# Performance work log

Measured on AMD Instinct MI355X. Metric: run time of the kernel, lower is better.

## Reference

```python
import jax, jax.numpy as jnp
import numpy as np

N, E, F, H, C = 50000, 800000, 64, 64, 10


def setup_inputs() -> dict:
    key = jax.random.key(0)
    ks = jax.random.split(key, 9)
    x = jax.random.normal(ks[0], (N, F), dtype=jnp.float32)
    edge_index = jax.random.randint(ks[1], (2, E), 0, N, dtype=jnp.int64)
    s_f = 1.0 / np.sqrt(F)
    s_h = 1.0 / np.sqrt(H)
    return {
        "x": x,
        "edge_index": edge_index,
        # ChebConv(F->H, K=1): only Theta_0
        "W1_0": jax.random.normal(ks[2], (F, H), dtype=jnp.float32) * s_f,
        "b1": jnp.zeros((H,), dtype=jnp.float32),
        # ChebConv(H->H, K=2): Theta_0, Theta_1
        "W2_0": jax.random.normal(ks[3], (H, H), dtype=jnp.float32) * s_h,
        "W2_1": jax.random.normal(ks[4], (H, H), dtype=jnp.float32) * s_h,
        "b2": jnp.zeros((H,), dtype=jnp.float32),
        # final Linear(H->C)
        "Wl": jax.random.normal(ks[5], (H, C), dtype=jnp.float32) * s_h,
        "bl": jnp.zeros((C,), dtype=jnp.float32),
    }


def reference(x, edge_index, W1_0, b1, W2_0, W2_1, b2, Wl, bl):
    n = x.shape[0]
    src, dst = edge_index[0], edge_index[1]
    # Scaled Laplacian (PyG ChebConv, sym norm, lambda_max=2.0):
    # L_hat = -D^{-1/2} A D^{-1/2}  (self-loop terms cancel: +1 scaled, then -1 added)
    deg = jax.ops.segment_sum(jnp.ones((src.shape[0],), dtype=x.dtype), src,
                              num_segments=n)
    dis = jnp.where(deg > 0, jax.lax.rsqrt(jnp.maximum(deg, 1.0)), 0.0)
    w = -(dis[src] * dis[dst])  # [E]

    def lap(h):  # L_hat @ h via edge-wise gather/scatter
        return jax.ops.segment_sum(w[:, None] * h[src], dst, num_segments=n)

    # conv1 (K=1): T0 = x only -> plain linear
    h = jax.nn.relu(x @ W1_0 + b1)
    # dropout is identity in eval mode
    x_res = h
    # conv2 (K=2): T0 = h, T1 = L_hat h
    h2 = jax.nn.relu(h @ W2_0 + lap(h) @ W2_1 + b2)
    out = (h2 + x_res) @ Wl + bl
    return jax.nn.log_softmax(out, axis=1)
```

## Files before the change

kernel.cpp:

```cpp
#include <hip/hip_runtime.h>
#include <math.h>
#include <stdint.h>


#define NBKT 256
#define BCAP 5120
#define CHUNK 2048

__device__ __forceinline__ unsigned short f2bf(float f) {
    uint32_t u; __builtin_memcpy(&u, &f, 4);
    u += 0x7fffu + ((u >> 16) & 1u);
    return (unsigned short)(u >> 16);
}
__device__ __forceinline__ float bf2f(unsigned short s) {
    uint32_t u = (uint32_t)s << 16; float f; __builtin_memcpy(&f, &u, 4);
    return f;
}
__device__ __forceinline__ int xcc_id() {
    int x;
    asm("s_getreg_b32 %0, hwreg(HW_REG_XCC_ID)" : "=s"(x));
    return x;
}

__global__ __launch_bounds__(256) void binA_kernel(const int* __restrict__ ei,
                                                   int* __restrict__ gcur,
                                                   uint32_t* __restrict__ pairs,
                                                   int* __restrict__ degI8,
                                                   int E, int n) {
    __shared__ uint32_t stage[CHUNK];
    __shared__ int cnt[NBKT], obase[NBKT], goff[NBKT], curs[NBKT];
    __shared__ int wpart[4], stot;
    int t = threadIdx.x, lane = t & 63, wv = t >> 6;
    int e0 = blockIdx.x * CHUNK;
    int* degP = degI8 + (size_t)(xcc_id() & 7) * n;
    int s[8], d[8];
    bool val[8];
#pragma unroll
    for (int j = 0; j < 8; ++j) {
        int e = e0 + j * 256 + t;
        val[j] = e < E;
        s[j] = val[j] ? ei[e] : 0;
        d[j] = val[j] ? ei[E + e] : 0;
    }
    cnt[t] = 0;
    __syncthreads();
#pragma unroll
    for (int j = 0; j < 8; ++j)
        if (val[j]) {
            atomicAdd(&cnt[d[j] >> 8], 1);
            atomicAdd(&degP[s[j]], 1);
        }
    __syncthreads();
    int cv = cnt[t];
    int v = cv;
#pragma unroll
    for (int dd = 1; dd < 64; dd <<= 1) {
        int u = __shfl_up(v, dd);
        if (lane >= dd) v += u;
    }
    if (lane == 63) wpart[wv] = v;
    __syncthreads();
    if (t == 0) {
        int r = 0;
#pragma unroll
        for (int w = 0; w < 4; ++w) { int tmp = wpart[w]; wpart[w] = r; r += tmp; }
        stot = r;
    }
    __syncthreads();
    int eb = wpart[wv] + v - cv;
    obase[t] = eb;
    curs[t] = eb;
    goff[t] = (cv > 0) ? atomicAdd(&gcur[t], cv) : 0;
    __syncthreads();
#pragma unroll
    for (int j = 0; j < 8; ++j)
        if (val[j]) {
            int b = d[j] >> 8;
            int pos = atomicAdd(&curs[b], 1);
            stage[pos] = ((uint32_t)d[j] << 16) | (uint32_t)s[j];
        }
    __syncthreads();
    int tot = stot;
    for (int k = t; k < tot; k += 256) {
        uint32_t u = stage[k];
        int b = (int)(u >> 24);
        int slot = goff[b] + (k - obase[b]);
        if (slot < BCAP) pairs[(size_t)b * BCAP + slot] = u;
    }
}

__global__ __launch_bounds__(256) void binB_kernel(const int* __restrict__ gcur,
                                                   const uint32_t* __restrict__ pairs,
                                                   int* __restrict__ csr,
                                                   int* __restrict__ rowptr,
                                                   int* __restrict__ cntD,
                                                   int* __restrict__ cntLow,
                                                   const int* __restrict__ degI8,
                                                   float* __restrict__ dis,
                                                   int n, int half) {
    __shared__ int hist[NBKT], obase[NBKT], cursL[NBKT], cursH[NBKT];
    __shared__ int wpart[4];
    int t = threadIdx.x, lane = t & 63, wv = t >> 6;
    int b = blockIdx.x;
    {
        int node = b * 256 + t;
        if (node < n) {
            int dsum = 0;
#pragma unroll
            for (int j = 0; j < 8; ++j) dsum += degI8[(size_t)j * n + node];
            dis[node] = (dsum > 0) ? rsqrtf((float)dsum) : 0.0f;
        }
    }
    int nb = gcur[b]; if (nb > BCAP) nb = BCAP;
    hist[t] = 0;
    __syncthreads();
    const uint32_t* bp = pairs + (size_t)b * BCAP;
    for (int k = t; k < nb; k += 256) {
        int ld = (int)((bp[k] >> 16) & 255);
        atomicAdd(&hist[ld], 1);
    }
    __syncthreads();
    int cv = hist[t];
    int v = cv;
#pragma unroll
    for (int dd = 1; dd < 64; dd <<= 1) {
        int u = __shfl_up(v, dd);
        if (lane >= dd) v += u;
    }
    if (lane == 63) wpart[wv] = v;
    __syncthreads();
    if (t == 0) {
        int r = 0;
#pragma unroll
        for (int w = 0; w < 4; ++w) { int tmp = wpart[w]; wpart[w] = r; r += tmp; }
    }
    __syncthreads();
    int eb = wpart[wv] + v - cv;
    obase[t] = eb;
    cursL[t] = eb;
    cursH[t] = eb + cv;
    int node = b * 256 + t;
    if (node < n) {
        rowptr[node] = b * BCAP + eb;
        cntD[node] = cv;
    }
    __syncthreads();
    for (int k = t; k < nb; k += 256) {
        uint32_t u = bp[k];
        int ld = (int)((u >> 16) & 255);
        int src = (int)(u & 0xffffu);
        int pos;
        if (src < half) pos = atomicAdd(&cursL[ld], 1);
        else            pos = atomicSub(&cursH[ld], 1) - 1;
        csr[(size_t)b * BCAP + pos] = src;
    }
    __syncthreads();
    if (node < n) cntLow[node] = cursL[t] - obase[t];
}

__global__ __launch_bounds__(256) void gemm3_kernel(const float* __restrict__ x,
                                                    const float* __restrict__ W1,
                                                    const float* __restrict__ b1,
                                                    const float* __restrict__ W20,
                                                    const float* __restrict__ W21,
                                                    const float* __restrict__ b2,
                                                    const float* __restrict__ dis,
                                                    unsigned short* __restrict__ h16,
                                                    unsigned short* __restrict__ p16,
                                                    unsigned short* __restrict__ g16,
                                                    int n) {
    __shared__ __align__(16) float sA[64][68];
    __shared__ __align__(16) float sW1[64][64];
    __shared__ __align__(16) float sW20[64][64];
    __shared__ __align__(16) float sW21[64][64];
    int t = threadIdx.x;
    for (int i = t; i < 4096; i += 256) {
        sW1[i >> 6][i & 63] = W1[i];
        sW20[i >> 6][i & 63] = W20[i];
        sW21[i >> 6][i & 63] = W21[i];
    }
    int r0 = blockIdx.x * 64;
    {
        int rr0 = t >> 4, k0 = (t & 15) * 4;
        for (int rr = rr0; rr < 64; rr += 16) {
            int grow = r0 + rr;
            float4 v = make_float4(0.f, 0.f, 0.f, 0.f);
            if (grow < n) v = *(const float4*)&x[(size_t)grow * 64 + k0];
            sA[k0][rr] = v.x; sA[k0 + 1][rr] = v.y;
            sA[k0 + 2][rr] = v.z; sA[k0 + 3][rr] = v.w;
        }
    }
    __syncthreads();
    int tr = t >> 4, tc = t & 15;

    float acc[4][4] = {};
    for (int k = 0; k < 64; ++k) {
        float4 a = *(const float4*)&sA[k][tr * 4];
        float4 b = *(const float4*)&sW1[k][tc * 4];
        float av[4] = {a.x, a.y, a.z, a.w};
        float bv[4] = {b.x, b.y, b.z, b.w};
#pragma unroll
        for (int i = 0; i < 4; ++i)
#pragma unroll
            for (int j = 0; j < 4; ++j) acc[i][j] = fmaf(av[i], bv[j], acc[i][j]);
    }
    float4 bv1 = *(const float4*)&b1[tc * 4];
    float hv[4][4];
#pragma unroll
    for (int i = 0; i < 4; ++i) {
        hv[i][0] = fmaxf(acc[i][0] + bv1.x, 0.f);
        hv[i][1] = fmaxf(acc[i][1] + bv1.y, 0.f);
        hv[i][2] = fmaxf(acc[i][2] + bv1.z, 0.f);
        hv[i][3] = fmaxf(acc[i][3] + bv1.w, 0.f);
    }
#pragma unroll
    for (int i = 0; i < 4; ++i) {
        int grow = r0 + tr * 4 + i;
        if (grow < n) {
            ushort4 o;
            o.x = f2bf(hv[i][0]); o.y = f2bf(hv[i][1]);
            o.z = f2bf(hv[i][2]); o.w = f2bf(hv[i][3]);
            *(ushort4*)&h16[(size_t)grow * 64 + tc * 4] = o;
        }
    }
    __syncthreads();
#pragma unroll
    for (int i = 0; i < 4; ++i)
#pragma unroll
        for (int j = 0; j < 4; ++j) sA[tc * 4 + j][tr * 4 + i] = hv[i][j];
    __syncthreads();

    float accP[4][4] = {}, accG[4][4] = {};
    for (int k = 0; k < 64; ++k) {
        float4 a = *(const float4*)&sA[k][tr * 4];
        float4 bp = *(const float4*)&sW20[k][tc * 4];
        float4 bg = *(const float4*)&sW21[k][tc * 4];
        float av[4] = {a.x, a.y, a.z, a.w};
        float bpv[4] = {bp.x, bp.y, bp.z, bp.w};
        float bgv[4] = {bg.x, bg.y, bg.z, bg.w};
#pragma unroll
        for (int i = 0; i < 4; ++i)
#pragma unroll
            for (int j = 0; j < 4; ++j) {
                accP[i][j] = fmaf(av[i], bpv[j], accP[i][j]);
                accG[i][j] = fmaf(av[i], bgv[j], accG[i][j]);
            }
    }
    float4 bv2 = *(const float4*)&b2[tc * 4];
#pragma unroll
    for (int i = 0; i < 4; ++i) {
        int grow = r0 + tr * 4 + i;
        if (grow < n) {
            float dr = dis[grow];
            ushort4 op, og;
            op.x = f2bf(accP[i][0] + bv2.x); op.y = f2bf(accP[i][1] + bv2.y);
            op.z = f2bf(accP[i][2] + bv2.z); op.w = f2bf(accP[i][3] + bv2.w);
            og.x = f2bf(dr * accG[i][0]); og.y = f2bf(dr * accG[i][1]);
            og.z = f2bf(dr * accG[i][2]); og.w = f2bf(dr * accG[i][3]);
            *(ushort4*)&p16[(size_t)grow * 64 + tc * 4] = op;
            *(ushort4*)&g16[(size_t)grow * 64 + tc * 4] = og;
        }
    }
}

#define GATHER_SEG(K0, K1)                                                  \
    {                                                                        \
        int k = (K0);                                                        \
        for (; k + 16 <= (K1); k += 16) {                                    \
            int s0 = csr[rs + k],      s1 = csr[rs + k + 1];                 \
            int s2 = csr[rs + k + 2],  s3 = csr[rs + k + 3];                 \
            int s4 = csr[rs + k + 4],  s5 = csr[rs + k + 5];                 \
            int s6 = csr[rs + k + 6],  s7 = csr[rs + k + 7];                 \
            int s8 = csr[rs + k + 8],  s9 = csr[rs + k + 9];                 \
            int sa = csr[rs + k + 10], sb = csr[rs + k + 11];                \
            int sc = csr[rs + k + 12], sd = csr[rs + k + 13];                \
            int se = csr[rs + k + 14], sf = csr[rs + k + 15];                \
            float v0 = bf2f(g16[(size_t)s0 * 64 + c]);                       \
            float v1 = bf2f(g16[(size_t)s1 * 64 + c]);                       \
            float v2 = bf2f(g16[(size_t)s2 * 64 + c]);                       \
            float v3 = bf2f(g16[(size_t)s3 * 64 + c]);                       \
            float v4 = bf2f(g16[(size_t)s4 * 64 + c]);                       \
            float v5 = bf2f(g16[(size_t)s5 * 64 + c]);                       \
            float v6 = bf2f(g16[(size_t)s6 * 64 + c]);                       \
            float v7 = bf2f(g16[(size_t)s7 * 64 + c]);                       \
            float v8 = bf2f(g16[(size_t)s8 * 64 + c]);                       \
            float v9 = bf2f(g16[(size_t)s9 * 64 + c]);                       \
            float va = bf2f(g16[(size_t)sa * 64 + c]);                       \
            float vb = bf2f(g16[(size_t)sb * 64 + c]);                       \
            float vc = bf2f(g16[(size_t)sc * 64 + c]);                       \
            float vd = bf2f(g16[(size_t)sd * 64 + c]);                       \
            float ve = bf2f(g16[(size_t)se * 64 + c]);                       \
            float vf = bf2f(g16[(size_t)sf * 64 + c]);                       \
            a0 += v0 + v8; a1 += v1 + v9; a2 += v2 + va; a3 += v3 + vb;      \
            a4 += v4 + vc; a5 += v5 + vd; a6 += v6 + ve; a7 += v7 + vf;      \
        }                                                                    \
        for (; k + 4 <= (K1); k += 4) {                                      \
            int s0 = csr[rs + k],     s1 = csr[rs + k + 1];                  \
            int s2 = csr[rs + k + 2], s3 = csr[rs + k + 3];                  \
            a0 += bf2f(g16[(size_t)s0 * 64 + c]);                            \
            a1 += bf2f(g16[(size_t)s1 * 64 + c]);                            \
            a2 += bf2f(g16[(size_t)s2 * 64 + c]);                            \
            a3 += bf2f(g16[(size_t)s3 * 64 + c]);                            \
        }                                                                    \
        for (; k < (K1); ++k) {                                              \
            int s0 = csr[rs + k];                                            \
            a0 += bf2f(g16[(size_t)s0 * 64 + c]);                            \
        }                                                                    \
    }

__global__ __launch_bounds__(256, 8) void gather_out_kernel(
        const int* __restrict__ rowptr, const int* __restrict__ cntD,
        const int* __restrict__ cntLow, const int* __restrict__ csr,
        const float* __restrict__ dis,
        const unsigned short* __restrict__ g16, const unsigned short* __restrict__ p16,
        const unsigned short* __restrict__ h16, const float* __restrict__ Wl,
        const float* __restrict__ bl, float* __restrict__ out, int n) {
    __shared__ __align__(16) float so[4][68];
    __shared__ __align__(16) float sWlT[10][68];
    __shared__ float sout[4][12];
    int t = threadIdx.x;
    if (t < 160) {
        float4 w = *(const float4*)&Wl[t * 4];
        int i0 = t * 4;
        sWlT[i0 % 10][i0 / 10] = w.x;
        sWlT[(i0 + 1) % 10][(i0 + 1) / 10] = w.y;
        sWlT[(i0 + 2) % 10][(i0 + 2) / 10] = w.z;
        sWlT[(i0 + 3) % 10][(i0 + 3) / 10] = w.w;
    }
    int c = t & 63;
    int wid = __builtin_amdgcn_readfirstlane(t >> 6);
    int row = blockIdx.x * 4 + wid;
    if (row < n) {
        int m = cntD[row], rs = rowptr[row], mL = cntLow[row];
        float disd = dis[row];
        float a0 = 0.f, a1 = 0.f, a2 = 0.f, a3 = 0.f;
        float a4 = 0.f, a5 = 0.f, a6 = 0.f, a7 = 0.f;
        GATHER_SEG(0, mL);
        GATHER_SEG(mL, m);
        float lv = -disd * (((a0 + a1) + (a2 + a3)) + ((a4 + a5) + (a6 + a7)));
        float pv = bf2f(p16[(size_t)row * 64 + c]);
        float hv = bf2f(h16[(size_t)row * 64 + c]);
        so[wid][c] = fmaxf(pv + lv, 0.f) + hv;
    }
    __syncthreads();
    if (t < 40) {
        int r = t / 10, j = t % 10;
        float acc = bl[j];
#pragma unroll
        for (int k0 = 0; k0 < 64; k0 += 4) {
            float4 a = *(const float4*)&so[r][k0];
            float4 b = *(const float4*)&sWlT[j][k0];
            acc = fmaf(a.x, b.x, acc);
            acc = fmaf(a.y, b.y, acc);
            acc = fmaf(a.z, b.z, acc);
            acc = fmaf(a.w, b.w, acc);
        }
        sout[r][j] = acc;
    }
    __syncthreads();
    if (t < 64) {
        int r = t >> 4, l16 = t & 15;
        float v = (l16 < 10) ? sout[r][l16] : -1e30f;
        float mm = v;
#pragma unroll
        for (int d = 1; d < 16; d <<= 1) mm = fmaxf(mm, __shfl_xor(mm, d, 16));
        float e = (l16 < 10) ? expf(v - mm) : 0.f;
        float ss = e;
#pragma unroll
        for (int d = 1; d < 16; d <<= 1) ss += __shfl_xor(ss, d, 16);
        int grow = blockIdx.x * 4 + r;
        if (grow < n && l16 < 10)
            out[(size_t)grow * 10 + l16] = v - mm - logf(ss);
    }
}

extern "C" void kernel_launch(void* const* d_in, const int* in_sizes, int n_in,
                              void* d_out, int out_size, void* d_ws, size_t ws_size,
                              hipStream_t stream) {
    const float* x   = (const float*)d_in[0];
    const int*   ei  = (const int*)d_in[1];
    const float* W1  = (const float*)d_in[2];
    const float* b1  = (const float*)d_in[3];
    const float* W20 = (const float*)d_in[4];
    const float* W21 = (const float*)d_in[5];
    const float* b2  = (const float*)d_in[6];
    const float* Wl  = (const float*)d_in[7];
    const float* bl  = (const float*)d_in[8];
    float* out = (float*)d_out;

    int n = in_sizes[0] / 64;
    int E = in_sizes[1] / 2;

    char* ws = (char*)d_ws;
    size_t off = 0;
    auto alloc = [&](size_t bytes) {
        void* p = ws + off;
        off = (off + bytes + 255) & ~(size_t)255;
        return p;
    };
    int*       gcur   = (int*)alloc((size_t)NBKT * 4);
    uint32_t*  pairs  = (uint32_t*)alloc((size_t)NBKT * BCAP * 4);
    int*       csr    = (int*)alloc((size_t)NBKT * BCAP * 4);
    int*       rowptr = (int*)alloc((size_t)n * 4);
    int*       cntD   = (int*)alloc((size_t)n * 4);
    int*       cntLow = (int*)alloc((size_t)n * 4);
    int*       degI8  = (int*)alloc((size_t)n * 8 * 4);
    float*     dis    = (float*)alloc((size_t)n * 4);
    unsigned short* h16 = (unsigned short*)alloc((size_t)n * 64 * 2);
    unsigned short* p16 = (unsigned short*)alloc((size_t)n * 64 * 2);
    unsigned short* g16 = (unsigned short*)alloc((size_t)n * 64 * 2);

    hipMemsetAsync(gcur, 0, (size_t)NBKT * 4, stream);
    hipMemsetAsync(degI8, 0, (size_t)n * 8 * 4, stream);

    int nchunk = (E + CHUNK - 1) / CHUNK;
    binA_kernel<<<nchunk, 256, 0, stream>>>(ei, gcur, pairs, degI8, E, n);
    binB_kernel<<<NBKT, 256, 0, stream>>>(gcur, pairs, csr, rowptr, cntD, cntLow,
                                          degI8, dis, n, n / 2);
    gemm3_kernel<<<(n + 63) / 64, 256, 0, stream>>>(x, W1, b1, W20, W21, b2, dis,
                                                    h16, p16, g16, n);
    gather_out_kernel<<<(n + 3) / 4, 256, 0, stream>>>(rowptr, cntD, cntLow, csr,
                                                       dis, g16, p16, h16, Wl, bl,
                                                       out, n);
}
```

Baseline: 198.5 us.

## Gather two bf16 features per lane with half-waves splitting edges

The gather kernel now reads packed bf16 pairs as 32-bit words, so each half-wave covers a full 64-feature row. The two half-waves process alternating edges and combine their sums with a cross-lane shuffle. This halves the number of load instructions per edge and doubles the edges in flight per wave. The low/high source split in CSR construction (cntLow, the two-ended cursors) is dropped in favour of a single cursor, which gives up the locality ordering of source indices that the split provided.

```diff
diff --git a/kernel.cpp b/kernel.cpp
--- a/kernel.cpp
+++ b/kernel.cpp
@@ -15,6 +15,12 @@
 __device__ __forceinline__ float bf2f(unsigned short s) {
     uint32_t u = (uint32_t)s << 16; float f; __builtin_memcpy(&f, &u, 4);
     return f;
+}
+__device__ __forceinline__ float lo_of(uint32_t u) {
+    uint32_t v = u << 16; float f; __builtin_memcpy(&f, &v, 4); return f;
+}
+__device__ __forceinline__ float hi_of(uint32_t u) {
+    uint32_t v = u & 0xffff0000u; float f; __builtin_memcpy(&f, &v, 4); return f;
 }
 __device__ __forceinline__ int xcc_id() {
     int x;
@@ -94,11 +100,9 @@
                                                    int* __restrict__ csr,
                                                    int* __restrict__ rowptr,
                                                    int* __restrict__ cntD,
-                                                   int* __restrict__ cntLow,
                                                    const int* __restrict__ degI8,
-                                                   float* __restrict__ dis,
-                                                   int n, int half) {
-    __shared__ int hist[NBKT], obase[NBKT], cursL[NBKT], cursH[NBKT];
+                                                   float* __restrict__ dis, int n) {
+    __shared__ int hist[NBKT], obase[NBKT], curs[NBKT];
     __shared__ int wpart[4];
     int t = threadIdx.x, lane = t & 63, wv = t >> 6;
     int b = blockIdx.x;
@@ -137,8 +141,7 @@
     __syncthreads();
     int eb = wpart[wv] + v - cv;
     obase[t] = eb;
-    cursL[t] = eb;
-    cursH[t] = eb + cv;
+    curs[t] = eb;
     int node = b * 256 + t;
     if (node < n) {
         rowptr[node] = b * BCAP + eb;
@@ -148,14 +151,9 @@
     for (int k = t; k < nb; k += 256) {
         uint32_t u = bp[k];
         int ld = (int)((u >> 16) & 255);
-        int src = (int)(u & 0xffffu);
-        int pos;
-        if (src < half) pos = atomicAdd(&cursL[ld], 1);
-        else            pos = atomicSub(&cursH[ld], 1) - 1;
-        csr[(size_t)b * BCAP + pos] = src;
-    }
-    __syncthreads();
-    if (node < n) cntLow[node] = cursL[t] - obase[t];
+        int pos = atomicAdd(&curs[ld], 1);
+        csr[(size_t)b * BCAP + pos] = (int)(u & 0xffffu);
+    }
 }
 
 __global__ __launch_bounds__(256) void gemm3_kernel(const float* __restrict__ x,
@@ -263,57 +261,11 @@
     }
 }
 
-#define GATHER_SEG(K0, K1)                                                  \
-    {                                                                        \
-        int k = (K0);                                                        \
-        for (; k + 16 <= (K1); k += 16) {                                    \
-            int s0 = csr[rs + k],      s1 = csr[rs + k + 1];                 \
-            int s2 = csr[rs + k + 2],  s3 = csr[rs + k + 3];                 \
-            int s4 = csr[rs + k + 4],  s5 = csr[rs + k + 5];                 \
-            int s6 = csr[rs + k + 6],  s7 = csr[rs + k + 7];                 \
-            int s8 = csr[rs + k + 8],  s9 = csr[rs + k + 9];                 \
-            int sa = csr[rs + k + 10], sb = csr[rs + k + 11];                \
-            int sc = csr[rs + k + 12], sd = csr[rs + k + 13];                \
-            int se = csr[rs + k + 14], sf = csr[rs + k + 15];                \
-            float v0 = bf2f(g16[(size_t)s0 * 64 + c]);                       \
-            float v1 = bf2f(g16[(size_t)s1 * 64 + c]);                       \
-            float v2 = bf2f(g16[(size_t)s2 * 64 + c]);                       \
-            float v3 = bf2f(g16[(size_t)s3 * 64 + c]);                       \
-            float v4 = bf2f(g16[(size_t)s4 * 64 + c]);                       \
-            float v5 = bf2f(g16[(size_t)s5 * 64 + c]);                       \
-            float v6 = bf2f(g16[(size_t)s6 * 64 + c]);                       \
-            float v7 = bf2f(g16[(size_t)s7 * 64 + c]);                       \
-            float v8 = bf2f(g16[(size_t)s8 * 64 + c]);                       \
-            float v9 = bf2f(g16[(size_t)s9 * 64 + c]);                       \
-            float va = bf2f(g16[(size_t)sa * 64 + c]);                       \
-            float vb = bf2f(g16[(size_t)sb * 64 + c]);                       \
-            float vc = bf2f(g16[(size_t)sc * 64 + c]);                       \
-            float vd = bf2f(g16[(size_t)sd * 64 + c]);                       \
-            float ve = bf2f(g16[(size_t)se * 64 + c]);                       \
-            float vf = bf2f(g16[(size_t)sf * 64 + c]);                       \
-            a0 += v0 + v8; a1 += v1 + v9; a2 += v2 + va; a3 += v3 + vb;      \
-            a4 += v4 + vc; a5 += v5 + vd; a6 += v6 + ve; a7 += v7 + vf;      \
-        }                                                                    \
-        for (; k + 4 <= (K1); k += 4) {                                      \
-            int s0 = csr[rs + k],     s1 = csr[rs + k + 1];                  \
-            int s2 = csr[rs + k + 2], s3 = csr[rs + k + 3];                  \
-            a0 += bf2f(g16[(size_t)s0 * 64 + c]);                            \
-            a1 += bf2f(g16[(size_t)s1 * 64 + c]);                            \
-            a2 += bf2f(g16[(size_t)s2 * 64 + c]);                            \
-            a3 += bf2f(g16[(size_t)s3 * 64 + c]);                            \
-        }                                                                    \
-        for (; k < (K1); ++k) {                                              \
-            int s0 = csr[rs + k];                                            \
-            a0 += bf2f(g16[(size_t)s0 * 64 + c]);                            \
-        }                                                                    \
-    }
-
 __global__ __launch_bounds__(256, 8) void gather_out_kernel(
         const int* __restrict__ rowptr, const int* __restrict__ cntD,
-        const int* __restrict__ cntLow, const int* __restrict__ csr,
-        const float* __restrict__ dis,
-        const unsigned short* __restrict__ g16, const unsigned short* __restrict__ p16,
-        const unsigned short* __restrict__ h16, const float* __restrict__ Wl,
+        const int* __restrict__ csr, const float* __restrict__ dis,
+        const uint32_t* __restrict__ gp, const uint32_t* __restrict__ pp,
+        const uint32_t* __restrict__ hp, const float* __restrict__ Wl,
         const float* __restrict__ bl, float* __restrict__ out, int n) {
     __shared__ __align__(16) float so[4][68];
     __shared__ __align__(16) float sWlT[10][68];
@@ -327,20 +279,75 @@
         sWlT[(i0 + 2) % 10][(i0 + 2) / 10] = w.z;
         sWlT[(i0 + 3) % 10][(i0 + 3) / 10] = w.w;
     }
-    int c = t & 63;
+    int p = t & 31;
+    int eslot = (t >> 5) & 1;
     int wid = __builtin_amdgcn_readfirstlane(t >> 6);
     int row = blockIdx.x * 4 + wid;
     if (row < n) {
-        int m = cntD[row], rs = rowptr[row], mL = cntLow[row];
+        int m = cntD[row], rs = rowptr[row];
         float disd = dis[row];
-        float a0 = 0.f, a1 = 0.f, a2 = 0.f, a3 = 0.f;
-        float a4 = 0.f, a5 = 0.f, a6 = 0.f, a7 = 0.f;
-        GATHER_SEG(0, mL);
-        GATHER_SEG(mL, m);
-        float lv = -disd * (((a0 + a1) + (a2 + a3)) + ((a4 + a5) + (a6 + a7)));
-        float pv = bf2f(p16[(size_t)row * 64 + c]);
-        float hv = bf2f(h16[(size_t)row * 64 + c]);
-        so[wid][c] = fmaxf(pv + lv, 0.f) + hv;
+        float l0 = 0.f, l1 = 0.f, l2 = 0.f, l3 = 0.f;
+        float h0 = 0.f, h1 = 0.f, h2a = 0.f, h3 = 0.f;
+        int k = 0;
+        for (; k + 16 <= m; k += 16) {
+            int sA0 = csr[rs + k + 0],  sA1 = csr[rs + k + 1];
+            int sA2 = csr[rs + k + 2],  sA3 = csr[rs + k + 3];
+            int sA4 = csr[rs + k + 4],  sA5 = csr[rs + k + 5];
+            int sA6 = csr[rs + k + 6],  sA7 = csr[rs + k + 7];
+            int sA8 = csr[rs + k + 8],  sA9 = csr[rs + k + 9];
+            int sAa = csr[rs + k + 10], sAb = csr[rs + k + 11];
+            int sAc = csr[rs + k + 12], sAd = csr[rs + k + 13];
+            int sAe = csr[rs + k + 14], sAf = csr[rs + k + 15];
+            int e0 = eslot ? sA1 : sA0;
+            int e1 = eslot ? sA3 : sA2;
+            int e2 = eslot ? sA5 : sA4;
+            int e3 = eslot ? sA7 : sA6;
+            int e4 = eslot ? sA9 : sA8;
+            int e5 = eslot ? sAb : sAa;
+            int e6 = eslot ? sAd : sAc;
+            int e7 = eslot ? sAf : sAe;
+            uint32_t u0 = gp[(size_t)e0 * 32 + p];
+            uint32_t u1 = gp[(size_t)e1 * 32 + p];
+            uint32_t u2 = gp[(size_t)e2 * 32 + p];
+            uint32_t u3 = gp[(size_t)e3 * 32 + p];
+            uint32_t u4 = gp[(size_t)e4 * 32 + p];
+            uint32_t u5 = gp[(size_t)e5 * 32 + p];
+            uint32_t u6 = gp[(size_t)e6 * 32 + p];
+            uint32_t u7 = gp[(size_t)e7 * 32 + p];
+            l0 += lo_of(u0); h0 += hi_of(u0);
+            l1 += lo_of(u1); h1 += hi_of(u1);
+            l2 += lo_of(u2); h2a += hi_of(u2);
+            l3 += lo_of(u3); h3 += hi_of(u3);
+            l0 += lo_of(u4); h0 += hi_of(u4);
+            l1 += lo_of(u5); h1 += hi_of(u5);
+            l2 += lo_of(u6); h2a += hi_of(u6);
+            l3 += lo_of(u7); h3 += hi_of(u7);
+        }
+        for (; k + 2 <= m; k += 2) {
+            int s0 = csr[rs + k], s1 = csr[rs + k + 1];
+            int e = eslot ? s1 : s0;
+            uint32_t u = gp[(size_t)e * 32 + p];
+            l0 += lo_of(u); h0 += hi_of(u);
+        }
+        if (k < m) {
+            int s0 = csr[rs + k];
+            if (eslot == 0) {
+                uint32_t u = gp[(size_t)s0 * 32 + p];
+                l0 += lo_of(u); h0 += hi_of(u);
+            }
+        }
+        float alo = (l0 + l1) + (l2 + l3);
+        float ahi = (h0 + h1) + (h2a + h3);
+        alo += __shfl_xor(alo, 32);
+        ahi += __shfl_xor(ahi, 32);
+        uint32_t up = pp[(size_t)row * 32 + p];
+        uint32_t uh = hp[(size_t)row * 32 + p];
+        float h2lo = fmaxf(lo_of(up) - disd * alo, 0.f) + lo_of(uh);
+        float h2hi = fmaxf(hi_of(up) - disd * ahi, 0.f) + hi_of(uh);
+        if (eslot == 0) {
+            so[wid][2 * p] = h2lo;
+            so[wid][2 * p + 1] = h2hi;
+        }
     }
     __syncthreads();
     if (t < 40) {
@@ -403,7 +410,6 @@
     int*       csr    = (int*)alloc((size_t)NBKT * BCAP * 4);
     int*       rowptr = (int*)alloc((size_t)n * 4);
     int*       cntD   = (int*)alloc((size_t)n * 4);
-    int*       cntLow = (int*)alloc((size_t)n * 4);
     int*       degI8  = (int*)alloc((size_t)n * 8 * 4);
     float*     dis    = (float*)alloc((size_t)n * 4);
     unsigned short* h16 = (unsigned short*)alloc((size_t)n * 64 * 2);
@@ -415,11 +421,12 @@
 
     int nchunk = (E + CHUNK - 1) / CHUNK;
     binA_kernel<<<nchunk, 256, 0, stream>>>(ei, gcur, pairs, degI8, E, n);
-    binB_kernel<<<NBKT, 256, 0, stream>>>(gcur, pairs, csr, rowptr, cntD, cntLow,
-                                          degI8, dis, n, n / 2);
+    binB_kernel<<<NBKT, 256, 0, stream>>>(gcur, pairs, csr, rowptr, cntD, degI8, dis, n);
     gemm3_kernel<<<(n + 63) / 64, 256, 0, stream>>>(x, W1, b1, W20, W21, b2, dis,
                                                     h16, p16, g16, n);
-    gather_out_kernel<<<(n + 3) / 4, 256, 0, stream>>>(rowptr, cntD, cntLow, csr,
-                                                       dis, g16, p16, h16, Wl, bl,
-                                                       out, n);
-}
+    gather_out_kernel<<<(n + 3) / 4, 256, 0, stream>>>(rowptr, cntD, csr, dis,
+                                                       (const uint32_t*)g16,
+                                                       (const uint32_t*)p16,
+                                                       (const uint32_t*)h16,
+                                                       Wl, bl, out, n);
+}
```

After: 194.0 us. 2.3% less time.
